# Kernel tuning notes

Hardware: AMD Instinct MI355X
Metric: run time of the kernel (lower is better)

Reference implementation:

```python
import jax, jax.numpy as jnp
import numpy as np
from jax import lax

STRIDE = 2
PAD = 1
EPS = 1e-6
K = 2  # top-k experts
E = 4  # num_experts
B, C1, H, W = 32, 64, 64, 64
C2 = 128
PATCH = 3


def conv_ln(x, w, b, gamma, beta):
    # Conv2d(c1->c2, patch, stride, pad) followed by channel-first LayerNorm
    y = lax.conv_general_dilated(x, w, (STRIDE, STRIDE), ((PAD, PAD), (PAD, PAD)),
                                 dimension_numbers=('NCHW', 'OIHW', 'NCHW'))
    y = y + b[None, :, None, None]
    u = y.mean(1, keepdims=True)
    s = ((y - u) ** 2).mean(1, keepdims=True)
    y = (y - u) / jnp.sqrt(s + EPS)
    return gamma[None, :, None, None] * y + beta[None, :, None, None]


def setup_inputs() -> dict:
    key = jax.random.key(0)
    ks = jax.random.split(key, 10)
    x = jax.random.normal(ks[0], (B, C1, H, W), dtype=jnp.float32)
    w_gate = jax.random.normal(ks[1], (C1, E), dtype=jnp.float32) * 0.02
    expert_w = jax.random.normal(ks[2], (E, C2, C1, PATCH, PATCH), dtype=jnp.float32) * 0.05
    expert_b = jax.random.normal(ks[3], (E, C2), dtype=jnp.float32) * 0.01
    expert_ln_w = jnp.ones((E, C2), dtype=jnp.float32)
    expert_ln_b = jnp.zeros((E, C2), dtype=jnp.float32)
    shared_w = jax.random.normal(ks[4], (C2, C1, PATCH, PATCH), dtype=jnp.float32) * 0.05
    shared_b = jax.random.normal(ks[5], (C2,), dtype=jnp.float32) * 0.01
    shared_ln_w = jnp.ones((C2,), dtype=jnp.float32)
    shared_ln_b = jnp.zeros((C2,), dtype=jnp.float32)
    return {"x": x, "w_gate": w_gate,
            "expert_w": expert_w, "expert_b": expert_b,
            "expert_ln_w": expert_ln_w, "expert_ln_b": expert_ln_b,
            "shared_w": shared_w, "shared_b": shared_b,
            "shared_ln_w": shared_ln_w, "shared_ln_b": shared_ln_b}


def reference(x, w_gate, expert_w, expert_b, expert_ln_w, expert_ln_b,
              shared_w, shared_b, shared_ln_w, shared_ln_b):
    # --- noisy top-k gating (eval mode: no noise) ---
    gate_in = x.mean(axis=(2, 3))            # [B, width]
    logits = gate_in @ w_gate                # [B, E]
    top_vals, top_idx = lax.top_k(logits, K) # [B, K]
    top_gates = jax.nn.softmax(top_vals, axis=-1)
    # scatter top-k gate values back to dense [B, E] gate matrix
    gates = jnp.sum(jax.nn.one_hot(top_idx, E, dtype=x.dtype) * top_gates[..., None], axis=1)
    # --- per-expert conv+LN; dense-weighted combine is math-equivalent to
    #     SparseDispatcher dispatch -> expert -> weighted index_add combine ---
    expert_out = jax.vmap(lambda w, b, g, bt: conv_ln(x, w, b, g, bt))(
        expert_w, expert_b, expert_ln_w, expert_ln_b)   # [E, B, C2, H', W']
    combined = jnp.einsum('be,ebchw->bchw', gates, expert_out)
    # --- shared expert added to routed output ---
    shared = conv_ln(x, shared_w, shared_b, shared_ln_w, shared_ln_b)
    return combined + shared
```

## Files before the change

### kernel.cpp

```cpp
#include <hip/hip_runtime.h>
#include <cstdint>
#include <cstddef>

#define NB    32
#define NC1   64
#define NC2   128
#define NE    4
#define NSLOT 5
#define HIN   64
#define WIN   64
#define HOUT  32
#define WOUT  32

#define GATEIN_OFF 0
#define GATES_OFF  2048
#define BIAS_OFF   2176
#define GAMMA_OFF  2816
#define BETA_OFF   3456
#define WBF_OFF    4096

typedef __bf16 bf16x8 __attribute__((ext_vector_type(8)));
typedef float  f32x16 __attribute__((ext_vector_type(16)));

__global__ void prep2_kernel(const float* __restrict__ x,
                             const float* __restrict__ expert_w,
                             const float* __restrict__ shared_w,
                             const float* __restrict__ expert_b,
                             const float* __restrict__ shared_b,
                             const float* __restrict__ eln_w,
                             const float* __restrict__ sln_w,
                             const float* __restrict__ eln_b,
                             const float* __restrict__ sln_b,
                             float* __restrict__ ws) {
    int bid = blockIdx.x;
    if (bid < 1440) {
        int i = bid * 256 + threadIdx.x;
        {
            int j    = i & 7;
            int l    = (i >> 3) & 63;
            int kk   = (i >> 9) & 3;
            int wv   = (i >> 11) & 3;
            int rest = i >> 13;
            int tap  = rest % 9;
            int e    = rest / 9;
            int c2 = wv * 32 + (l & 31);
            int c  = kk * 16 + (l >> 5) * 8 + j;
            float v;
            if (e < NE) v = expert_w[(((size_t)(e * NC2 + c2) * NC1 + c) * 9) + tap];
            else        v = shared_w[(((size_t)c2 * NC1 + c) * 9) + tap];
            ((__bf16*)(ws + WBF_OFF))[i] = (__bf16)v;
        }
        if (i < NSLOT * NC2) {
            int e = i >> 7, c2 = i & 127;
            ws[BIAS_OFF  + i] = (e < NE) ? expert_b[i] : shared_b[c2];
            ws[GAMMA_OFF + i] = (e < NE) ? eln_w[i]    : sln_w[c2];
            ws[BETA_OFF  + i] = (e < NE) ? eln_b[i]    : sln_b[c2];
        }
    } else {
        int row  = (bid - 1440) * 4 + (threadIdx.x >> 6);
        int lane = threadIdx.x & 63;
        const float* src = x + (size_t)row * (HIN * WIN);
        float s = 0.f;
        for (int i = lane * 4; i < HIN * WIN; i += 64 * 4) {
            float4 v = *(const float4*)(src + i);
            s += v.x + v.y + v.z + v.w;
        }
        #pragma unroll
        for (int off = 32; off >= 1; off >>= 1) s += __shfl_xor(s, off);
        if (lane == 0) ws[GATEIN_OFF + row] = s * (1.f / (HIN * WIN));
    }
}

__global__ void gate_kernel(const float* __restrict__ w_gate, float* __restrict__ ws) {
    int b = threadIdx.x;
    if (b >= NB) return;
    const float* gi = ws + GATEIN_OFF + b * NC1;
    float l[NE] = {0.f, 0.f, 0.f, 0.f};
    for (int c = 0; c < NC1; ++c) {
        float v = gi[c];
        #pragma unroll
        for (int e = 0; e < NE; ++e) l[e] += v * w_gate[c * NE + e];
    }
    int i0 = 0; float v0 = l[0];
    #pragma unroll
    for (int e = 1; e < NE; ++e) if (l[e] > v0) { v0 = l[e]; i0 = e; }
    int i1 = -1; float v1 = -3.4e38f;
    #pragma unroll
    for (int e = 0; e < NE; ++e) if (e != i0 && l[e] > v1) { v1 = l[e]; i1 = e; }
    float e1 = expf(v1 - v0);
    float denom = 1.f + e1;
    float g0 = 1.f / denom, g1 = e1 / denom;
    #pragma unroll
    for (int e = 0; e < NE; ++e)
        ws[GATES_OFF + b * NE + e] = (e == i0) ? g0 : ((e == i1) ? g1 : 0.f);
}

#define XS_IDX(r, p, ps, c7) ((((r) * 65 + (p)) << 6) + ((ps) << 3) + (c7))

__global__ __launch_bounds__(512, 4) void fused_kernel(
        const float* __restrict__ x,
        const float* __restrict__ ws,
        float* __restrict__ out) {
    __shared__ __bf16 xs[5 * 65 * 64];
    __shared__ float  red[6 * 2 * 128];

    const int bid = blockIdx.x;
    const int b   = bid >> 4;
    const int hg  = bid & 15;
    const int tid = threadIdx.x;
    const int ln  = tid & 63;
    const int wv8 = tid >> 6;
    const int t   = wv8 >> 2;
    const int wv  = wv8 & 3;
    const int cl  = ln & 31;
    const int hl  = ln >> 5;
    const int wbase = wv * 32;

    #pragma unroll
    for (int r = 0; r < 5; ++r) {
        const int hin = 4 * hg - 1 + r;
        #pragma unroll
        for (int pass = 0; pass < 2; ++pass) {
            int idx = (pass << 9) + tid;
            int c   = idx >> 4;
            int i4  = idx & 15;
            float4 v = make_float4(0.f, 0.f, 0.f, 0.f);
            if (hin >= 0)
                v = *(const float4*)(x + (((size_t)b * NC1 + c) * HIN + hin) * WIN + i4 * 4);
            #pragma unroll
            for (int k = 0; k < 4; ++k) {
                int p  = i4 * 4 + k + 1;
                int ps = (c >> 3) ^ ((p >> 1) & 7);
                float f = (k == 0) ? v.x : (k == 1) ? v.y : (k == 2) ? v.z : v.w;
                xs[XS_IDX(r, p, ps, c & 7)] = (__bf16)f;
            }
        }
    }
    if (tid < 64) {
        #pragma unroll
        for (int r = 0; r < 5; ++r) xs[XS_IDX(r, 0, (tid >> 3), tid & 7)] = (__bf16)0.f;
    }

    const float* gp = ws + GATES_OFF + b * NE;
    int s0 = -1, s1 = -1; float ga = 0.f, gb = 0.f;
    #pragma unroll
    for (int e = 0; e < NE; ++e) {
        float ge = gp[e];
        if (ge > 0.f) { if (s0 < 0) { s0 = e; ga = ge; } else if (s1 < 0) { s1 = e; gb = ge; } }
    }
    if (s0 < 0) { s0 = 0; ga = 0.f; }
    if (s1 < 0) { s1 = (s0 == 0) ? 1 : 0; gb = 0.f; }

    const int rowbase = wbase + 4 * hl;
    f32x16 acc0, acc1, acc2;
    #define INIT_ACC(ACC, SID)                                                  \
    {                                                                           \
        const float4* bp = (const float4*)(ws + BIAS_OFF + (SID) * NC2 + rowbase); \
        float4 b0 = bp[0], b1 = bp[2], b2 = bp[4], b3 = bp[6];                  \
        ACC[0]=b0.x; ACC[1]=b0.y; ACC[2]=b0.z; ACC[3]=b0.w;                     \
        ACC[4]=b1.x; ACC[5]=b1.y; ACC[6]=b1.z; ACC[7]=b1.w;                     \
        ACC[8]=b2.x; ACC[9]=b2.y; ACC[10]=b2.z; ACC[11]=b2.w;                   \
        ACC[12]=b3.x; ACC[13]=b3.y; ACC[14]=b3.z; ACC[15]=b3.w;                 \
    }
    INIT_ACC(acc0, s0) INIT_ACC(acc1, s1) INIT_ACC(acc2, 4)

    __syncthreads();

    const __bf16* wA = (const __bf16*)(ws + WBF_OFF);
    const int p_l = 2 * cl;
    const int rofs = 2 * t;
    #define MFMA(A, B, C) C = __builtin_amdgcn_mfma_f32_32x32x16_bf16(A, B, C, 0, 0, 0)
    #define DO_TAP(R_, KW_)                                                        \
    {                                                                              \
        const int tap = (R_) * 3 + (KW_);                                          \
        const int p   = p_l + (KW_);                                              \
        const int swb = (p >> 1) & 7;                                              \
        const __bf16* ap0 = wA + (((size_t)s0 * 9 + tap) * 4 + wv) * 2048 + ln * 8; \
        const __bf16* ap1 = wA + (((size_t)s1 * 9 + tap) * 4 + wv) * 2048 + ln * 8; \
        const __bf16* ap2 = wA + (((size_t)4  * 9 + tap) * 4 + wv) * 2048 + ln * 8; \
        _Pragma("unroll")                                                          \
        for (int kk = 0; kk < 4; ++kk) {                                           \
            bf16x8 bb = *(const bf16x8*)&xs[XS_IDX((R_) + rofs, p, (2 * kk + hl) ^ swb, 0)]; \
            bf16x8 a0 = *(const bf16x8*)(ap0 + kk * 512);                          \
            bf16x8 a1 = *(const bf16x8*)(ap1 + kk * 512);                          \
            bf16x8 a2 = *(const bf16x8*)(ap2 + kk * 512);                          \
            MFMA(a0, bb, acc0);                                                    \
            MFMA(a1, bb, acc1);                                                    \
            MFMA(a2, bb, acc2);                                                    \
        }                                                                          \
    }
    DO_TAP(0, 0) DO_TAP(0, 1) DO_TAP(0, 2)
    DO_TAP(1, 0) DO_TAP(1, 1) DO_TAP(1, 2)
    DO_TAP(2, 0) DO_TAP(2, 1) DO_TAP(2, 2)

    #define PUT_RED(ACC, SI)                                                      \
    {                                                                             \
        float sum = 0.f, sq = 0.f;                                                \
        _Pragma("unroll")                                                         \
        for (int i = 0; i < 16; ++i) { float a = ACC[i]; sum += a; sq += a * a; } \
        sum += __shfl_xor(sum, 32); sq += __shfl_xor(sq, 32);                     \
        if (ln < 32) {                                                            \
            red[(((SI) * 2 + t) * 2 + 0) * 128 + wbase + cl] = sum;               \
            red[(((SI) * 2 + t) * 2 + 1) * 128 + wbase + cl] = sq;                \
        }                                                                         \
    }
    PUT_RED(acc0, 0)
    PUT_RED(acc1, 1)
    PUT_RED(acc2, 2)
    __syncthreads();

    float fin[16];
    #pragma unroll
    for (int i = 0; i < 16; ++i) fin[i] = 0.f;

    #define APPLY(ACC, SI, GM, BT, G)                                             \
    {                                                                             \
        float tot = 0.f, totq = 0.f;                                              \
        _Pragma("unroll")                                                         \
        for (int w = 0; w < 4; ++w) {                                             \
            tot  += red[(((SI) * 2 + t) * 2 + 0) * 128 + w * 32 + cl];            \
            totq += red[(((SI) * 2 + t) * 2 + 1) * 128 + w * 32 + cl];            \
        }                                                                         \
        float mean = tot * (1.f / NC2);                                           \
        float var  = totq * (1.f / NC2) - mean * mean;                            \
        float rstd = rsqrtf(var + 1e-6f);                                         \
        _Pragma("unroll")                                                         \
        for (int i = 0; i < 16; ++i) {                                            \
            float nrm = (ACC[i] - mean) * rstd;                                   \
            fin[i] = fmaf((G), fmaf(GM[i], nrm, BT[i]), fin[i]);                  \
        }                                                                         \
    }
    #define LOAD_GB(SID, GM, BT)                                                  \
        float GM[16], BT[16];                                                     \
        {                                                                         \
            const float4* gmp = (const float4*)(ws + GAMMA_OFF + (SID) * NC2 + rowbase); \
            const float4* btp = (const float4*)(ws + BETA_OFF  + (SID) * NC2 + rowbase); \
            float4 g0 = gmp[0], g1 = gmp[2], g2 = gmp[4], g3 = gmp[6];            \
            float4 t0 = btp[0], t1 = btp[2], t2 = btp[4], t3 = btp[6];            \
            GM[0]=g0.x;GM[1]=g0.y;GM[2]=g0.z;GM[3]=g0.w;GM[4]=g1.x;GM[5]=g1.y;GM[6]=g1.z;GM[7]=g1.w; \
            GM[8]=g2.x;GM[9]=g2.y;GM[10]=g2.z;GM[11]=g2.w;GM[12]=g3.x;GM[13]=g3.y;GM[14]=g3.z;GM[15]=g3.w; \
            BT[0]=t0.x;BT[1]=t0.y;BT[2]=t0.z;BT[3]=t0.w;BT[4]=t1.x;BT[5]=t1.y;BT[6]=t1.z;BT[7]=t1.w; \
            BT[8]=t2.x;BT[9]=t2.y;BT[10]=t2.z;BT[11]=t2.w;BT[12]=t3.x;BT[13]=t3.y;BT[14]=t3.z;BT[15]=t3.w; \
        }
    {
        LOAD_GB(s0, gm0, bt0)
        APPLY(acc0, 0, gm0, bt0, ga)
    }
    {
        LOAD_GB(s1, gm1, bt1)
        APPLY(acc1, 1, gm1, bt1, gb)
    }
    {
        LOAD_GB(4, gm2, bt2)
        APPLY(acc2, 2, gm2, bt2, 1.0f)
    }

    {
        float* ob = out + (size_t)b * (NC2 * HOUT * WOUT) + (2 * hg + t) * WOUT + cl;
        #pragma unroll
        for (int i = 0; i < 16; ++i) {
            int c2 = rowbase + (i & 3) + 8 * (i >> 2);
            ob[(size_t)c2 * (HOUT * WOUT)] = fin[i];
        }
    }
}

extern "C" void kernel_launch(void* const* d_in, const int* in_sizes, int n_in,
                              void* d_out, int out_size, void* d_ws, size_t ws_size,
                              hipStream_t stream) {
    const float* x        = (const float*)d_in[0];
    const float* w_gate   = (const float*)d_in[1];
    const float* expert_w = (const float*)d_in[2];
    const float* expert_b = (const float*)d_in[3];
    const float* eln_w    = (const float*)d_in[4];
    const float* eln_b    = (const float*)d_in[5];
    const float* shared_w = (const float*)d_in[6];
    const float* shared_b = (const float*)d_in[7];
    const float* sln_w    = (const float*)d_in[8];
    const float* sln_b    = (const float*)d_in[9];
    float* ws  = (float*)d_ws;
    float* out = (float*)d_out;

    prep2_kernel<<<1952, 256, 0, stream>>>(x, expert_w, shared_w, expert_b, shared_b,
                                           eln_w, sln_w, eln_b, sln_b, ws);
    gate_kernel<<<1, 64, 0, stream>>>(w_gate, ws);
    fused_kernel<<<NB * 16, 512, 0, stream>>>(x, ws, out);
}
```

Baseline: 48.03 us.

## Fold gating into fused kernel and split experts across wave groups

Removes the separate single-block gate kernel by computing the top-2 gating per batch inside each fused block with a wave reduction. The block grows from 512 to 768 threads so each group of four waves handles one expert slot (two routed, one shared) over both output rows, reusing each weight fragment for two MFMAs instead of loading three weight streams per wave. Partial results are combined in shared memory across the wave groups and written out with coalesced float4 stores. This costs extra barriers and redundant gate computation per block, and the higher thread count puts more pressure on registers.

```diff
diff --git a/kernel.cpp b/kernel.cpp
--- a/kernel.cpp
+++ b/kernel.cpp
@@ -13,7 +13,6 @@
 #define WOUT  32
 
 #define GATEIN_OFF 0
-#define GATES_OFF  2048
 #define BIAS_OFF   2176
 #define GAMMA_OFF  2816
 #define BETA_OFF   3456
@@ -71,197 +70,193 @@
     }
 }
 
-__global__ void gate_kernel(const float* __restrict__ w_gate, float* __restrict__ ws) {
-    int b = threadIdx.x;
-    if (b >= NB) return;
-    const float* gi = ws + GATEIN_OFF + b * NC1;
-    float l[NE] = {0.f, 0.f, 0.f, 0.f};
-    for (int c = 0; c < NC1; ++c) {
-        float v = gi[c];
-        #pragma unroll
-        for (int e = 0; e < NE; ++e) l[e] += v * w_gate[c * NE + e];
-    }
-    int i0 = 0; float v0 = l[0];
-    #pragma unroll
-    for (int e = 1; e < NE; ++e) if (l[e] > v0) { v0 = l[e]; i0 = e; }
-    int i1 = -1; float v1 = -3.4e38f;
-    #pragma unroll
-    for (int e = 0; e < NE; ++e) if (e != i0 && l[e] > v1) { v1 = l[e]; i1 = e; }
-    float e1 = expf(v1 - v0);
-    float denom = 1.f + e1;
-    float g0 = 1.f / denom, g1 = e1 / denom;
-    #pragma unroll
-    for (int e = 0; e < NE; ++e)
-        ws[GATES_OFF + b * NE + e] = (e == i0) ? g0 : ((e == i1) ? g1 : 0.f);
-}
-
 #define XS_IDX(r, p, ps, c7) ((((r) * 65 + (p)) << 6) + ((ps) << 3) + (c7))
 
-__global__ __launch_bounds__(512, 4) void fused_kernel(
+__global__ __launch_bounds__(768, 6) void fused_kernel(
         const float* __restrict__ x,
+        const float* __restrict__ w_gate,
         const float* __restrict__ ws,
         float* __restrict__ out) {
-    __shared__ __bf16 xs[5 * 65 * 64];
-    __shared__ float  red[6 * 2 * 128];
+    __shared__ __align__(16) unsigned char smem[5 * 65 * 64 * 2];
+    __shared__ float red[3 * 2 * 2 * 128];
+    __shared__ float gsh[4];
+
+    __bf16* xs = (__bf16*)smem;
 
     const int bid = blockIdx.x;
     const int b   = bid >> 4;
     const int hg  = bid & 15;
     const int tid = threadIdx.x;
     const int ln  = tid & 63;
-    const int wv8 = tid >> 6;
-    const int t   = wv8 >> 2;
-    const int wv  = wv8 & 3;
+    const int wid = tid >> 6;
+    const int sg  = wid >> 2;
+    const int wv  = wid & 3;
     const int cl  = ln & 31;
     const int hl  = ln >> 5;
     const int wbase = wv * 32;
 
+    for (int idx = tid; idx < 5 * 1024; idx += 768) {
+        int r   = idx >> 10;
+        int rem = idx & 1023;
+        int c   = rem >> 4;
+        int i4  = rem & 15;
+        int hin = 4 * hg - 1 + r;
+        float4 v = make_float4(0.f, 0.f, 0.f, 0.f);
+        if (hin >= 0)
+            v = *(const float4*)(x + (((size_t)b * NC1 + c) * HIN + hin) * WIN + i4 * 4);
+        #pragma unroll
+        for (int k = 0; k < 4; ++k) {
+            int p  = i4 * 4 + k + 1;
+            int ps = (c >> 3) ^ ((p >> 1) & 7);
+            float f = (k == 0) ? v.x : (k == 1) ? v.y : (k == 2) ? v.z : v.w;
+            xs[XS_IDX(r, p, ps, c & 7)] = (__bf16)f;
+        }
+    }
+    if (tid >= 768 - 64) {
+        int l = tid & 63;
+        #pragma unroll
+        for (int r = 0; r < 5; ++r) xs[XS_IDX(r, 0, (l >> 3), l & 7)] = (__bf16)0.f;
+    }
+
+    if (tid < 64) {
+        float gi = ws[GATEIN_OFF + b * NC1 + tid];
+        float l[NE];
+        #pragma unroll
+        for (int e = 0; e < NE; ++e) {
+            float p = gi * w_gate[tid * NE + e];
+            #pragma unroll
+            for (int off = 32; off >= 1; off >>= 1) p += __shfl_xor(p, off);
+            l[e] = p;
+        }
+        if (tid == 0) {
+            int i0 = 0; float v0 = l[0];
+            #pragma unroll
+            for (int e = 1; e < NE; ++e) if (l[e] > v0) { v0 = l[e]; i0 = e; }
+            int i1 = -1; float v1 = -3.4e38f;
+            #pragma unroll
+            for (int e = 0; e < NE; ++e) if (e != i0 && l[e] > v1) { v1 = l[e]; i1 = e; }
+            float e1 = expf(v1 - v0);
+            float denom = 1.f + e1;
+            gsh[0] = (float)i0; gsh[1] = 1.f / denom;
+            gsh[2] = (float)i1; gsh[3] = e1 / denom;
+        }
+    }
+
+    __syncthreads();
+
+    int slot; float g;
+    if (sg == 0)      { slot = (int)gsh[0]; g = gsh[1]; }
+    else if (sg == 1) { slot = (int)gsh[2]; g = gsh[3]; }
+    else              { slot = 4;           g = 1.0f;   }
+
+    const int rowbase = wbase + 4 * hl;
+    f32x16 accA, accB;
+    {
+        const float4* bp = (const float4*)(ws + BIAS_OFF + slot * NC2 + rowbase);
+        float4 b0 = bp[0], b1 = bp[2], b2 = bp[4], b3 = bp[6];
+        accA[0]=b0.x; accA[1]=b0.y; accA[2]=b0.z; accA[3]=b0.w;
+        accA[4]=b1.x; accA[5]=b1.y; accA[6]=b1.z; accA[7]=b1.w;
+        accA[8]=b2.x; accA[9]=b2.y; accA[10]=b2.z; accA[11]=b2.w;
+        accA[12]=b3.x; accA[13]=b3.y; accA[14]=b3.z; accA[15]=b3.w;
+        accB = accA;
+    }
+
+    const __bf16* apb = (const __bf16*)(ws + WBF_OFF)
+                        + (size_t)slot * 73728 + wv * 2048 + ln * 8;
+    const int p_l = 2 * cl;
+    #define MFMA(A, B, C) C = __builtin_amdgcn_mfma_f32_32x32x16_bf16(A, B, C, 0, 0, 0)
     #pragma unroll
-    for (int r = 0; r < 5; ++r) {
-        const int hin = 4 * hg - 1 + r;
-        #pragma unroll
-        for (int pass = 0; pass < 2; ++pass) {
-            int idx = (pass << 9) + tid;
-            int c   = idx >> 4;
-            int i4  = idx & 15;
-            float4 v = make_float4(0.f, 0.f, 0.f, 0.f);
-            if (hin >= 0)
-                v = *(const float4*)(x + (((size_t)b * NC1 + c) * HIN + hin) * WIN + i4 * 4);
-            #pragma unroll
-            for (int k = 0; k < 4; ++k) {
-                int p  = i4 * 4 + k + 1;
-                int ps = (c >> 3) ^ ((p >> 1) & 7);
-                float f = (k == 0) ? v.x : (k == 1) ? v.y : (k == 2) ? v.z : v.w;
-                xs[XS_IDX(r, p, ps, c & 7)] = (__bf16)f;
+    for (int r3 = 0; r3 < 3; ++r3) {
+        #pragma unroll
+        for (int kw = 0; kw < 3; ++kw) {
+            const int tap = r3 * 3 + kw;
+            const int p   = p_l + kw;
+            const int swb = (p >> 1) & 7;
+            const __bf16* ap = apb + tap * 8192;
+            #pragma unroll
+            for (int kk = 0; kk < 4; ++kk) {
+                bf16x8 av = *(const bf16x8*)(ap + kk * 512);
+                bf16x8 bA = *(const bf16x8*)&xs[XS_IDX(r3,     p, (2 * kk + hl) ^ swb, 0)];
+                bf16x8 bB = *(const bf16x8*)&xs[XS_IDX(r3 + 2, p, (2 * kk + hl) ^ swb, 0)];
+                MFMA(av, bA, accA);
+                MFMA(av, bB, accB);
             }
         }
     }
-    if (tid < 64) {
-        #pragma unroll
-        for (int r = 0; r < 5; ++r) xs[XS_IDX(r, 0, (tid >> 3), tid & 7)] = (__bf16)0.f;
-    }
-
-    const float* gp = ws + GATES_OFF + b * NE;
-    int s0 = -1, s1 = -1; float ga = 0.f, gb = 0.f;
-    #pragma unroll
-    for (int e = 0; e < NE; ++e) {
-        float ge = gp[e];
-        if (ge > 0.f) { if (s0 < 0) { s0 = e; ga = ge; } else if (s1 < 0) { s1 = e; gb = ge; } }
-    }
-    if (s0 < 0) { s0 = 0; ga = 0.f; }
-    if (s1 < 0) { s1 = (s0 == 0) ? 1 : 0; gb = 0.f; }
-
-    const int rowbase = wbase + 4 * hl;
-    f32x16 acc0, acc1, acc2;
-    #define INIT_ACC(ACC, SID)                                                  \
-    {                                                                           \
-        const float4* bp = (const float4*)(ws + BIAS_OFF + (SID) * NC2 + rowbase); \
-        float4 b0 = bp[0], b1 = bp[2], b2 = bp[4], b3 = bp[6];                  \
-        ACC[0]=b0.x; ACC[1]=b0.y; ACC[2]=b0.z; ACC[3]=b0.w;                     \
-        ACC[4]=b1.x; ACC[5]=b1.y; ACC[6]=b1.z; ACC[7]=b1.w;                     \
-        ACC[8]=b2.x; ACC[9]=b2.y; ACC[10]=b2.z; ACC[11]=b2.w;                   \
-        ACC[12]=b3.x; ACC[13]=b3.y; ACC[14]=b3.z; ACC[15]=b3.w;                 \
-    }
-    INIT_ACC(acc0, s0) INIT_ACC(acc1, s1) INIT_ACC(acc2, 4)
-
-    __syncthreads();
-
-    const __bf16* wA = (const __bf16*)(ws + WBF_OFF);
-    const int p_l = 2 * cl;
-    const int rofs = 2 * t;
-    #define MFMA(A, B, C) C = __builtin_amdgcn_mfma_f32_32x32x16_bf16(A, B, C, 0, 0, 0)
-    #define DO_TAP(R_, KW_)                                                        \
-    {                                                                              \
-        const int tap = (R_) * 3 + (KW_);                                          \
-        const int p   = p_l + (KW_);                                              \
-        const int swb = (p >> 1) & 7;                                              \
-        const __bf16* ap0 = wA + (((size_t)s0 * 9 + tap) * 4 + wv) * 2048 + ln * 8; \
-        const __bf16* ap1 = wA + (((size_t)s1 * 9 + tap) * 4 + wv) * 2048 + ln * 8; \
-        const __bf16* ap2 = wA + (((size_t)4  * 9 + tap) * 4 + wv) * 2048 + ln * 8; \
-        _Pragma("unroll")                                                          \
-        for (int kk = 0; kk < 4; ++kk) {                                           \
-            bf16x8 bb = *(const bf16x8*)&xs[XS_IDX((R_) + rofs, p, (2 * kk + hl) ^ swb, 0)]; \
-            bf16x8 a0 = *(const bf16x8*)(ap0 + kk * 512);                          \
-            bf16x8 a1 = *(const bf16x8*)(ap1 + kk * 512);                          \
-            bf16x8 a2 = *(const bf16x8*)(ap2 + kk * 512);                          \
-            MFMA(a0, bb, acc0);                                                    \
-            MFMA(a1, bb, acc1);                                                    \
-            MFMA(a2, bb, acc2);                                                    \
-        }                                                                          \
-    }
-    DO_TAP(0, 0) DO_TAP(0, 1) DO_TAP(0, 2)
-    DO_TAP(1, 0) DO_TAP(1, 1) DO_TAP(1, 2)
-    DO_TAP(2, 0) DO_TAP(2, 1) DO_TAP(2, 2)
-
-    #define PUT_RED(ACC, SI)                                                      \
+
+    #define PUT_RED(ACC, T)                                                       \
     {                                                                             \
         float sum = 0.f, sq = 0.f;                                                \
         _Pragma("unroll")                                                         \
         for (int i = 0; i < 16; ++i) { float a = ACC[i]; sum += a; sq += a * a; } \
         sum += __shfl_xor(sum, 32); sq += __shfl_xor(sq, 32);                     \
         if (ln < 32) {                                                            \
-            red[(((SI) * 2 + t) * 2 + 0) * 128 + wbase + cl] = sum;               \
-            red[(((SI) * 2 + t) * 2 + 1) * 128 + wbase + cl] = sq;                \
+            red[((sg * 2 + (T)) * 2 + 0) * 128 + wbase + cl] = sum;               \
+            red[((sg * 2 + (T)) * 2 + 1) * 128 + wbase + cl] = sq;                \
         }                                                                         \
     }
-    PUT_RED(acc0, 0)
-    PUT_RED(acc1, 1)
-    PUT_RED(acc2, 2)
-    __syncthreads();
-
-    float fin[16];
-    #pragma unroll
-    for (int i = 0; i < 16; ++i) fin[i] = 0.f;
-
-    #define APPLY(ACC, SI, GM, BT, G)                                             \
+    PUT_RED(accA, 0)
+    PUT_RED(accB, 1)
+    __syncthreads();
+
+    float vA[16], vB[16];
+    float gm[16], bt[16];
+    {
+        const float4* gmp = (const float4*)(ws + GAMMA_OFF + slot * NC2 + rowbase);
+        const float4* btp = (const float4*)(ws + BETA_OFF  + slot * NC2 + rowbase);
+        float4 g0 = gmp[0], g1 = gmp[2], g2 = gmp[4], g3 = gmp[6];
+        float4 t0 = btp[0], t1 = btp[2], t2 = btp[4], t3 = btp[6];
+        gm[0]=g0.x;gm[1]=g0.y;gm[2]=g0.z;gm[3]=g0.w;gm[4]=g1.x;gm[5]=g1.y;gm[6]=g1.z;gm[7]=g1.w;
+        gm[8]=g2.x;gm[9]=g2.y;gm[10]=g2.z;gm[11]=g2.w;gm[12]=g3.x;gm[13]=g3.y;gm[14]=g3.z;gm[15]=g3.w;
+        bt[0]=t0.x;bt[1]=t0.y;bt[2]=t0.z;bt[3]=t0.w;bt[4]=t1.x;bt[5]=t1.y;bt[6]=t1.z;bt[7]=t1.w;
+        bt[8]=t2.x;bt[9]=t2.y;bt[10]=t2.z;bt[11]=t2.w;bt[12]=t3.x;bt[13]=t3.y;bt[14]=t3.z;bt[15]=t3.w;
+    }
+    #define APPLY(ACC, OUT, T)                                                    \
     {                                                                             \
-        float tot = 0.f, totq = 0.f;                                              \
-        _Pragma("unroll")                                                         \
-        for (int w = 0; w < 4; ++w) {                                             \
-            tot  += red[(((SI) * 2 + t) * 2 + 0) * 128 + w * 32 + cl];            \
-            totq += red[(((SI) * 2 + t) * 2 + 1) * 128 + w * 32 + cl];            \
-        }                                                                         \
+        float tot  = red[((sg * 2 + (T)) * 2 + 0) * 128 + 0 * 32 + cl]            \
+                   + red[((sg * 2 + (T)) * 2 + 0) * 128 + 1 * 32 + cl]            \
+                   + red[((sg * 2 + (T)) * 2 + 0) * 128 + 2 * 32 + cl]            \
+                   + red[((sg * 2 + (T)) * 2 + 0) * 128 + 3 * 32 + cl];           \
+        float totq = red[((sg * 2 + (T)) * 2 + 1) * 128 + 0 * 32 + cl]            \
+                   + red[((sg * 2 + (T)) * 2 + 1) * 128 + 1 * 32 + cl]            \
+                   + red[((sg * 2 + (T)) * 2 + 1) * 128 + 2 * 32 + cl]            \
+                   + red[((sg * 2 + (T)) * 2 + 1) * 128 + 3 * 32 + cl];           \
         float mean = tot * (1.f / NC2);                                           \
         float var  = totq * (1.f / NC2) - mean * mean;                            \
         float rstd = rsqrtf(var + 1e-6f);                                         \
         _Pragma("unroll")                                                         \
         for (int i = 0; i < 16; ++i) {                                            \
             float nrm = (ACC[i] - mean) * rstd;                                   \
-            fin[i] = fmaf((G), fmaf(GM[i], nrm, BT[i]), fin[i]);                  \
+            OUT[i] = g * fmaf(gm[i], nrm, bt[i]);                                 \
         }                                                                         \
     }
-    #define LOAD_GB(SID, GM, BT)                                                  \
-        float GM[16], BT[16];                                                     \
-        {                                                                         \
-            const float4* gmp = (const float4*)(ws + GAMMA_OFF + (SID) * NC2 + rowbase); \
-            const float4* btp = (const float4*)(ws + BETA_OFF  + (SID) * NC2 + rowbase); \
-            float4 g0 = gmp[0], g1 = gmp[2], g2 = gmp[4], g3 = gmp[6];            \
-            float4 t0 = btp[0], t1 = btp[2], t2 = btp[4], t3 = btp[6];            \
-            GM[0]=g0.x;GM[1]=g0.y;GM[2]=g0.z;GM[3]=g0.w;GM[4]=g1.x;GM[5]=g1.y;GM[6]=g1.z;GM[7]=g1.w; \
-            GM[8]=g2.x;GM[9]=g2.y;GM[10]=g2.z;GM[11]=g2.w;GM[12]=g3.x;GM[13]=g3.y;GM[14]=g3.z;GM[15]=g3.w; \
-            BT[0]=t0.x;BT[1]=t0.y;BT[2]=t0.z;BT[3]=t0.w;BT[4]=t1.x;BT[5]=t1.y;BT[6]=t1.z;BT[7]=t1.w; \
-            BT[8]=t2.x;BT[9]=t2.y;BT[10]=t2.z;BT[11]=t2.w;BT[12]=t3.x;BT[13]=t3.y;BT[14]=t3.z;BT[15]=t3.w; \
-        }
-    {
-        LOAD_GB(s0, gm0, bt0)
-        APPLY(acc0, 0, gm0, bt0, ga)
-    }
-    {
-        LOAD_GB(s1, gm1, bt1)
-        APPLY(acc1, 1, gm1, bt1, gb)
-    }
-    {
-        LOAD_GB(4, gm2, bt2)
-        APPLY(acc2, 2, gm2, bt2, 1.0f)
-    }
-
-    {
-        float* ob = out + (size_t)b * (NC2 * HOUT * WOUT) + (2 * hg + t) * WOUT + cl;
-        #pragma unroll
-        for (int i = 0; i < 16; ++i) {
-            int c2 = rowbase + (i & 3) + 8 * (i >> 2);
-            ob[(size_t)c2 * (HOUT * WOUT)] = fin[i];
-        }
+    APPLY(accA, vA, 0)
+    APPLY(accB, vB, 1)
+
+    float* ob = (float*)smem;
+    #define OB_WR(OP)                                                             \
+    {                                                                             \
+        _Pragma("unroll")                                                         \
+        for (int i = 0; i < 16; ++i) {                                            \
+            int c2 = rowbase + (i & 3) + 8 * (i >> 2);                            \
+            ob[(0 * 128 + c2) * 32 + cl] OP vA[i];                                \
+            ob[(1 * 128 + c2) * 32 + cl] OP vB[i];                                \
+        }                                                                         \
+    }
+    if (sg == 0) OB_WR(=)
+    __syncthreads();
+    if (sg == 1) OB_WR(+=)
+    __syncthreads();
+    if (sg == 2) OB_WR(+=)
+    __syncthreads();
+
+    for (int idx = tid; idx < 2048; idx += 768) {
+        int t   = idx >> 10;
+        int rem = idx & 1023;
+        int c2  = rem >> 3;
+        int q   = rem & 7;
+        float4 v = *(const float4*)&ob[(t * 128 + c2) * 32 + q * 4];
+        *(float4*)(out + (((size_t)b * NC2 + c2) * HOUT + 2 * hg + t) * WOUT + q * 4) = v;
     }
 }
 
@@ -283,6 +278,5 @@
 
     prep2_kernel<<<1952, 256, 0, stream>>>(x, expert_w, shared_w, expert_b, shared_b,
                                            eln_w, sln_w, eln_b, sln_b, ws);
-    gate_kernel<<<1, 64, 0, stream>>>(w_gate, ws);
-    fused_kernel<<<NB * 16, 512, 0, stream>>>(x, ws, out);
+    fused_kernel<<<NB * 16, 768, 0, stream>>>(x, w_gate, ws, out);
 }
```

Result: slower. 73.98 us (+54.0%).

## Fold gating into fused kernel, double-buffer weights in LDS, stage output stores

Applied to the files above, without the earlier changes.

Removes the separate single-block gate kernel and computes top-2 gating per block with wave shuffles, which saves one launch and its serialization. Expert and shared weights for each conv tap are now prefetched into a double-buffered LDS region with global_load_lds, so the next tap's load overlaps the current tap's MFMAs instead of each wave reading A fragments straight from global memory. Output is staged through LDS so it can be written with coalesced float4 stores. The cost is much larger shared memory (occupancy hint drops from 4 to 2 blocks) and a __syncthreads per tap.

```diff
diff --git a/kernel.cpp b/kernel.cpp
--- a/kernel.cpp
+++ b/kernel.cpp
@@ -13,7 +13,6 @@
 #define WOUT  32
 
 #define GATEIN_OFF 0
-#define GATES_OFF  2048
 #define BIAS_OFF   2176
 #define GAMMA_OFF  2816
 #define BETA_OFF   3456
@@ -21,6 +20,11 @@
 
 typedef __bf16 bf16x8 __attribute__((ext_vector_type(8)));
 typedef float  f32x16 __attribute__((ext_vector_type(16)));
+
+#define GLOAD_LDS16(G, L)                                                        \
+    __builtin_amdgcn_global_load_lds(                                            \
+        (const __attribute__((address_space(1))) void*)(G),                      \
+        (__attribute__((address_space(3))) void*)(L), 16, 0, 0)
 
 __global__ void prep2_kernel(const float* __restrict__ x,
                              const float* __restrict__ expert_w,
@@ -71,38 +75,19 @@
     }
 }
 
-__global__ void gate_kernel(const float* __restrict__ w_gate, float* __restrict__ ws) {
-    int b = threadIdx.x;
-    if (b >= NB) return;
-    const float* gi = ws + GATEIN_OFF + b * NC1;
-    float l[NE] = {0.f, 0.f, 0.f, 0.f};
-    for (int c = 0; c < NC1; ++c) {
-        float v = gi[c];
-        #pragma unroll
-        for (int e = 0; e < NE; ++e) l[e] += v * w_gate[c * NE + e];
-    }
-    int i0 = 0; float v0 = l[0];
-    #pragma unroll
-    for (int e = 1; e < NE; ++e) if (l[e] > v0) { v0 = l[e]; i0 = e; }
-    int i1 = -1; float v1 = -3.4e38f;
-    #pragma unroll
-    for (int e = 0; e < NE; ++e) if (e != i0 && l[e] > v1) { v1 = l[e]; i1 = e; }
-    float e1 = expf(v1 - v0);
-    float denom = 1.f + e1;
-    float g0 = 1.f / denom, g1 = e1 / denom;
-    #pragma unroll
-    for (int e = 0; e < NE; ++e)
-        ws[GATES_OFF + b * NE + e] = (e == i0) ? g0 : ((e == i1) ? g1 : 0.f);
-}
-
 #define XS_IDX(r, p, ps, c7) ((((r) * 65 + (p)) << 6) + ((ps) << 3) + (c7))
-
-__global__ __launch_bounds__(512, 4) void fused_kernel(
+#define XS_BYTES   41600
+#define WBUF_ELEMS 24576
+
+__global__ __launch_bounds__(512, 2) void fused_kernel(
         const float* __restrict__ x,
+        const float* __restrict__ w_gate,
         const float* __restrict__ ws,
         float* __restrict__ out) {
-    __shared__ __bf16 xs[5 * 65 * 64];
-    __shared__ float  red[6 * 2 * 128];
+    __shared__ __align__(16) unsigned char smem[XS_BYTES + 2 * 49152 + 6144];
+    __bf16* xs  = (__bf16*)smem;
+    __bf16* wb  = (__bf16*)(smem + XS_BYTES);
+    float*  red = (float*)(smem + XS_BYTES + 2 * 49152);
 
     const int bid = blockIdx.x;
     const int b   = bid >> 4;
@@ -110,11 +95,50 @@
     const int tid = threadIdx.x;
     const int ln  = tid & 63;
     const int wv8 = tid >> 6;
-    const int t   = wv8 >> 2;
+    const int tg  = wv8 >> 2;
     const int wv  = wv8 & 3;
     const int cl  = ln & 31;
     const int hl  = ln >> 5;
     const int wbase = wv * 32;
+
+    int s0, s1; float ga, gb;
+    {
+        float gi = ws[GATEIN_OFF + b * NC1 + ln];
+        float l[NE];
+        #pragma unroll
+        for (int e = 0; e < NE; ++e) {
+            float p = gi * w_gate[ln * NE + e];
+            #pragma unroll
+            for (int off = 32; off >= 1; off >>= 1) p += __shfl_xor(p, off);
+            l[e] = p;
+        }
+        int i0 = 0; float v0 = l[0];
+        #pragma unroll
+        for (int e = 1; e < NE; ++e) if (l[e] > v0) { v0 = l[e]; i0 = e; }
+        int i1 = -1; float v1 = -3.4e38f;
+        #pragma unroll
+        for (int e = 0; e < NE; ++e) if (e != i0 && l[e] > v1) { v1 = l[e]; i1 = e; }
+        float e1 = expf(v1 - v0);
+        float denom = 1.f + e1;
+        s0 = i0; ga = 1.f / denom;
+        s1 = i1; gb = e1 / denom;
+    }
+
+    const __bf16* wtab = (const __bf16*)(ws + WBF_OFF);
+    #define ISSUE_W(TAP, BUF)                                                     \
+    {                                                                             \
+        _Pragma("unroll")                                                         \
+        for (int i = 0; i < 6; ++i) {                                             \
+            int chunk = wv8 * 6 + i;                     \
+            int si    = chunk >> 4;                            \
+            int off   = (chunk & 15) << 9;               \
+            int sl    = (si == 0) ? s0 : ((si == 1) ? s1 : 4);                    \
+            const __bf16* g = wtab + (size_t)sl * 73728 + (TAP) * 8192 + off + ln * 8; \
+            __bf16* d = wb + (BUF) * WBUF_ELEMS + si * 8192 + off;                \
+            GLOAD_LDS16(g, d);                                                    \
+        }                                                                         \
+    }
+    ISSUE_W(0, 0)
 
     #pragma unroll
     for (int r = 0; r < 5; ++r) {
@@ -141,16 +165,6 @@
         for (int r = 0; r < 5; ++r) xs[XS_IDX(r, 0, (tid >> 3), tid & 7)] = (__bf16)0.f;
     }
 
-    const float* gp = ws + GATES_OFF + b * NE;
-    int s0 = -1, s1 = -1; float ga = 0.f, gb = 0.f;
-    #pragma unroll
-    for (int e = 0; e < NE; ++e) {
-        float ge = gp[e];
-        if (ge > 0.f) { if (s0 < 0) { s0 = e; ga = ge; } else if (s1 < 0) { s1 = e; gb = ge; } }
-    }
-    if (s0 < 0) { s0 = 0; ga = 0.f; }
-    if (s1 < 0) { s1 = (s0 == 0) ? 1 : 0; gb = 0.f; }
-
     const int rowbase = wbase + 4 * hl;
     f32x16 acc0, acc1, acc2;
     #define INIT_ACC(ACC, SID)                                                  \
@@ -166,32 +180,29 @@
 
     __syncthreads();
 
-    const __bf16* wA = (const __bf16*)(ws + WBF_OFF);
+    #define MFMA(A, B, C) C = __builtin_amdgcn_mfma_f32_32x32x16_bf16(A, B, C, 0, 0, 0)
     const int p_l = 2 * cl;
-    const int rofs = 2 * t;
-    #define MFMA(A, B, C) C = __builtin_amdgcn_mfma_f32_32x32x16_bf16(A, B, C, 0, 0, 0)
-    #define DO_TAP(R_, KW_)                                                        \
-    {                                                                              \
-        const int tap = (R_) * 3 + (KW_);                                          \
-        const int p   = p_l + (KW_);                                              \
-        const int swb = (p >> 1) & 7;                                              \
-        const __bf16* ap0 = wA + (((size_t)s0 * 9 + tap) * 4 + wv) * 2048 + ln * 8; \
-        const __bf16* ap1 = wA + (((size_t)s1 * 9 + tap) * 4 + wv) * 2048 + ln * 8; \
-        const __bf16* ap2 = wA + (((size_t)4  * 9 + tap) * 4 + wv) * 2048 + ln * 8; \
-        _Pragma("unroll")                                                          \
-        for (int kk = 0; kk < 4; ++kk) {                                           \
-            bf16x8 bb = *(const bf16x8*)&xs[XS_IDX((R_) + rofs, p, (2 * kk + hl) ^ swb, 0)]; \
-            bf16x8 a0 = *(const bf16x8*)(ap0 + kk * 512);                          \
-            bf16x8 a1 = *(const bf16x8*)(ap1 + kk * 512);                          \
-            bf16x8 a2 = *(const bf16x8*)(ap2 + kk * 512);                          \
-            MFMA(a0, bb, acc0);                                                    \
-            MFMA(a1, bb, acc1);                                                    \
-            MFMA(a2, bb, acc2);                                                    \
-        }                                                                          \
-    }
-    DO_TAP(0, 0) DO_TAP(0, 1) DO_TAP(0, 2)
-    DO_TAP(1, 0) DO_TAP(1, 1) DO_TAP(1, 2)
-    DO_TAP(2, 0) DO_TAP(2, 1) DO_TAP(2, 2)
+    #pragma unroll
+    for (int t = 0; t < 9; ++t) {
+        if (t < 8) { ISSUE_W(t + 1, (t + 1) & 1) }
+        const int r3  = t / 3;
+        const int kw  = t % 3;
+        const int r   = r3 + 2 * tg;
+        const int p   = p_l + kw;
+        const int swb = (p >> 1) & 7;
+        const __bf16* wbc = wb + (t & 1) * WBUF_ELEMS + wv * 2048 + ln * 8;
+        #pragma unroll
+        for (int kk = 0; kk < 4; ++kk) {
+            bf16x8 bb = *(const bf16x8*)&xs[XS_IDX(r, p, (2 * kk + hl) ^ swb, 0)];
+            bf16x8 a0 = *(const bf16x8*)(wbc + 0 * 8192 + kk * 512);
+            bf16x8 a1 = *(const bf16x8*)(wbc + 1 * 8192 + kk * 512);
+            bf16x8 a2 = *(const bf16x8*)(wbc + 2 * 8192 + kk * 512);
+            MFMA(a0, bb, acc0);
+            MFMA(a1, bb, acc1);
+            MFMA(a2, bb, acc2);
+        }
+        __syncthreads();
+    }
 
     #define PUT_RED(ACC, SI)                                                      \
     {                                                                             \
@@ -200,8 +211,8 @@
         for (int i = 0; i < 16; ++i) { float a = ACC[i]; sum += a; sq += a * a; } \
         sum += __shfl_xor(sum, 32); sq += __shfl_xor(sq, 32);                     \
         if (ln < 32) {                                                            \
-            red[(((SI) * 2 + t) * 2 + 0) * 128 + wbase + cl] = sum;               \
-            red[(((SI) * 2 + t) * 2 + 1) * 128 + wbase + cl] = sq;                \
+            red[(((SI) * 2 + tg) * 2 + 0) * 128 + wbase + cl] = sum;              \
+            red[(((SI) * 2 + tg) * 2 + 1) * 128 + wbase + cl] = sq;               \
         }                                                                         \
     }
     PUT_RED(acc0, 0)
@@ -213,55 +224,49 @@
     #pragma unroll
     for (int i = 0; i < 16; ++i) fin[i] = 0.f;
 
-    #define APPLY(ACC, SI, GM, BT, G)                                             \
+    #define APPLY(ACC, SI, SID, G)                                                \
     {                                                                             \
         float tot = 0.f, totq = 0.f;                                              \
         _Pragma("unroll")                                                         \
         for (int w = 0; w < 4; ++w) {                                             \
-            tot  += red[(((SI) * 2 + t) * 2 + 0) * 128 + w * 32 + cl];            \
-            totq += red[(((SI) * 2 + t) * 2 + 1) * 128 + w * 32 + cl];            \
+            tot  += red[(((SI) * 2 + tg) * 2 + 0) * 128 + w * 32 + cl];           \
+            totq += red[(((SI) * 2 + tg) * 2 + 1) * 128 + w * 32 + cl];           \
         }                                                                         \
         float mean = tot * (1.f / NC2);                                           \
         float var  = totq * (1.f / NC2) - mean * mean;                            \
         float rstd = rsqrtf(var + 1e-6f);                                         \
+        const float4* gmp = (const float4*)(ws + GAMMA_OFF + (SID) * NC2 + rowbase); \
+        const float4* btp = (const float4*)(ws + BETA_OFF  + (SID) * NC2 + rowbase); \
+        float4 g0 = gmp[0], g1 = gmp[2], g2 = gmp[4], g3 = gmp[6];                \
+        float4 t0 = btp[0], t1 = btp[2], t2 = btp[4], t3 = btp[6];                \
+        float gm[16] = {g0.x,g0.y,g0.z,g0.w, g1.x,g1.y,g1.z,g1.w,                 \
+                        g2.x,g2.y,g2.z,g2.w, g3.x,g3.y,g3.z,g3.w};                \
+        float bt[16] = {t0.x,t0.y,t0.z,t0.w, t1.x,t1.y,t1.z,t1.w,                 \
+                        t2.x,t2.y,t2.z,t2.w, t3.x,t3.y,t3.z,t3.w};                \
         _Pragma("unroll")                                                         \
         for (int i = 0; i < 16; ++i) {                                            \
             float nrm = (ACC[i] - mean) * rstd;                                   \
-            fin[i] = fmaf((G), fmaf(GM[i], nrm, BT[i]), fin[i]);                  \
-        }                                                                         \
-    }
-    #define LOAD_GB(SID, GM, BT)                                                  \
-        float GM[16], BT[16];                                                     \
-        {                                                                         \
-            const float4* gmp = (const float4*)(ws + GAMMA_OFF + (SID) * NC2 + rowbase); \
-            const float4* btp = (const float4*)(ws + BETA_OFF  + (SID) * NC2 + rowbase); \
-            float4 g0 = gmp[0], g1 = gmp[2], g2 = gmp[4], g3 = gmp[6];            \
-            float4 t0 = btp[0], t1 = btp[2], t2 = btp[4], t3 = btp[6];            \
-            GM[0]=g0.x;GM[1]=g0.y;GM[2]=g0.z;GM[3]=g0.w;GM[4]=g1.x;GM[5]=g1.y;GM[6]=g1.z;GM[7]=g1.w; \
-            GM[8]=g2.x;GM[9]=g2.y;GM[10]=g2.z;GM[11]=g2.w;GM[12]=g3.x;GM[13]=g3.y;GM[14]=g3.z;GM[15]=g3.w; \
-            BT[0]=t0.x;BT[1]=t0.y;BT[2]=t0.z;BT[3]=t0.w;BT[4]=t1.x;BT[5]=t1.y;BT[6]=t1.z;BT[7]=t1.w; \
-            BT[8]=t2.x;BT[9]=t2.y;BT[10]=t2.z;BT[11]=t2.w;BT[12]=t3.x;BT[13]=t3.y;BT[14]=t3.z;BT[15]=t3.w; \
-        }
-    {
-        LOAD_GB(s0, gm0, bt0)
-        APPLY(acc0, 0, gm0, bt0, ga)
-    }
-    {
-        LOAD_GB(s1, gm1, bt1)
-        APPLY(acc1, 1, gm1, bt1, gb)
-    }
-    {
-        LOAD_GB(4, gm2, bt2)
-        APPLY(acc2, 2, gm2, bt2, 1.0f)
-    }
-
-    {
-        float* ob = out + (size_t)b * (NC2 * HOUT * WOUT) + (2 * hg + t) * WOUT + cl;
-        #pragma unroll
-        for (int i = 0; i < 16; ++i) {
-            int c2 = rowbase + (i & 3) + 8 * (i >> 2);
-            ob[(size_t)c2 * (HOUT * WOUT)] = fin[i];
-        }
+            fin[i] = fmaf((G), fmaf(gm[i], nrm, bt[i]), fin[i]);                  \
+        }                                                                         \
+    }
+    APPLY(acc0, 0, s0, ga)
+    APPLY(acc1, 1, s1, gb)
+    APPLY(acc2, 2, 4, 1.0f)
+
+    float* ob = (float*)(smem + XS_BYTES);
+    #pragma unroll
+    for (int i = 0; i < 16; ++i) {
+        int c2 = rowbase + (i & 3) + 8 * (i >> 2);
+        ob[(tg * 128 + c2) * 32 + cl] = fin[i];
+    }
+    __syncthreads();
+    for (int idx = tid; idx < 2048; idx += 512) {
+        int t2  = idx >> 10;
+        int rem = idx & 1023;
+        int c2  = rem >> 3;
+        int q   = rem & 7;
+        float4 v = *(const float4*)&ob[(t2 * 128 + c2) * 32 + q * 4];
+        *(float4*)(out + (((size_t)b * NC2 + c2) * HOUT + 2 * hg + t2) * WOUT + q * 4) = v;
     }
 }
 
@@ -283,6 +288,5 @@
 
     prep2_kernel<<<1952, 256, 0, stream>>>(x, expert_w, shared_w, expert_b, shared_b,
                                            eln_w, sln_w, eln_b, sln_b, ws);
-    gate_kernel<<<1, 64, 0, stream>>>(w_gate, ws);
-    fused_kernel<<<NB * 16, 512, 0, stream>>>(x, ws, out);
+    fused_kernel<<<NB * 16, 512, 0, stream>>>(x, w_gate, ws, out);
 }
```

New measurement: 47.26 us. About the same (-1.6%).
